# Kernel tuning notes

Hardware: AMD Instinct MI355X
Metric: run time of the kernel (lower is better)

Reference implementation:

```python
import jax, jax.numpy as jnp
import numpy as np

N, E, D, G, L = 100000, 1600000, 64, 512, 3
EPS = 1e-5


def setup_inputs() -> dict:
    key = jax.random.key(0)
    ks = jax.random.split(key, 8)
    x = jax.random.normal(ks[0], (N, D), dtype=jnp.float32)
    edge_index = jax.random.randint(ks[1], (2, E), 0, N, dtype=jnp.int32)
    batch = jnp.sort(jax.random.randint(ks[2], (N,), 0, G, dtype=jnp.int32))
    s = 1.0 / np.sqrt(D)
    convW = jax.random.normal(ks[3], (L, D, D), dtype=jnp.float32) * s
    convB = jnp.zeros((L, D), jnp.float32)
    bn_g = jnp.ones((L, D), jnp.float32); bn_b = jnp.zeros((L, D), jnp.float32)
    ln_g = jnp.ones((L, D), jnp.float32); ln_b = jnp.zeros((L, D), jnp.float32)
    W1 = jax.random.normal(ks[4], (3 * D, 2 * D), dtype=jnp.float32) * (1.0 / np.sqrt(3 * D))
    b1 = jnp.zeros((2 * D,), jnp.float32)
    ln1_g = jnp.ones((2 * D,), jnp.float32); ln1_b = jnp.zeros((2 * D,), jnp.float32)
    W2 = jax.random.normal(ks[5], (2 * D, D), dtype=jnp.float32) * (1.0 / np.sqrt(2 * D))
    b2 = jnp.zeros((D,), jnp.float32)
    ln2_g = jnp.ones((D,), jnp.float32); ln2_b = jnp.zeros((D,), jnp.float32)
    W3 = jax.random.normal(ks[6], (D, 1), dtype=jnp.float32) * s
    b3 = jnp.zeros((1,), jnp.float32)
    return dict(x=x, edge_index=edge_index, batch=batch, convW=convW, convB=convB,
                bn_g=bn_g, bn_b=bn_b, ln_g=ln_g, ln_b=ln_b,
                W1=W1, b1=b1, ln1_g=ln1_g, ln1_b=ln1_b,
                W2=W2, b2=b2, ln2_g=ln2_g, ln2_b=ln2_b, W3=W3, b3=b3)


def _layer_norm(h, g, b):
    mu = jnp.mean(h, axis=-1, keepdims=True)
    var = jnp.mean((h - mu) ** 2, axis=-1, keepdims=True)
    return (h - mu) * jax.lax.rsqrt(var + EPS) * g + b


def _forward(x, edge_index, batch, convW, convB, bn_g, bn_b, ln_g, ln_b,
             W1, b1, ln1_g, ln1_b, W2, b2, ln2_g, ln2_b, W3, b3):
    n = x.shape[0]
    loops = jnp.arange(n, dtype=edge_index.dtype)
    src = jnp.concatenate([edge_index[0], loops])  # self-loops as in GCNConv
    dst = jnp.concatenate([edge_index[1], loops])
    deg = jax.ops.segment_sum(jnp.ones_like(src, dtype=x.dtype), dst, num_segments=n)
    dinv = jnp.where(deg > 0, jax.lax.rsqrt(deg), 0.0)
    norm = (dinv[src] * dinv[dst])[:, None]  # [E+N, 1]

    h = x
    for i in range(L):
        x_in = h
        hw = h @ convW[i]                                   # [N, D]
        agg = jax.ops.segment_sum(norm * hw[src], dst, num_segments=n) + convB[i]
        # BatchNorm1d (train-mode batch stats, biased var)
        mu = jnp.mean(agg, axis=0)
        var = jnp.mean((agg - mu) ** 2, axis=0)
        hb = (agg - mu) * jax.lax.rsqrt(var + EPS) * bn_g[i] + bn_b[i]
        if i > 0:
            hb = hb + x_in  # residual (shapes match: D == D)
        h = jax.nn.gelu(_layer_norm(hb, ln_g[i], ln_b[i]), approximate=False)

    # multi-pool over graphs
    cnt = jax.ops.segment_sum(jnp.ones((n,), x.dtype), batch, num_segments=G)[:, None]
    s = jax.ops.segment_sum(h, batch, num_segments=G)
    mean = s / jnp.maximum(cnt, 1.0)
    mx = jax.ops.segment_max(h, batch, num_segments=G)
    mx = jnp.where(cnt > 0, mx, 0.0)
    z = jnp.concatenate([mean, mx, s], axis=1)  # [G, 3D]

    z = jax.nn.gelu(_layer_norm(z @ W1 + b1, ln1_g, ln1_b), approximate=False)
    z = jax.nn.gelu(_layer_norm(z @ W2 + b2, ln2_g, ln2_b), approximate=False)
    return z @ W3 + b3  # [G, num_classes]


def reference(x, edge_index, batch, convW, convB, bn_g, bn_b, ln_g, ln_b,
              W1, b1, ln1_g, ln1_b, W2, b2, ln2_g, ln2_b, W3, b3):
    return _forward(x, edge_index, batch, convW, convB, bn_g, bn_b, ln_g, ln_b,
                    W1, b1, ln1_g, ln1_b, W2, b2, ln2_g, ln2_b, W3, b3)
```

## Files before the change

kernel.cpp:

```cpp
#include <hip/hip_runtime.h>
#include <hip/hip_bf16.h>
#include <hip/hip_fp16.h>

#define DD 64
#define EPSV 1e-5f
#define NSLICE 16

typedef __attribute__((ext_vector_type(4))) _Float16 f16x4;
typedef __attribute__((ext_vector_type(8))) _Float16 f16x8;
typedef __attribute__((ext_vector_type(4))) float f32x4;

static __device__ __forceinline__ float fatomic_add(float* p, float v) {
#if defined(__HIP_DEVICE_COMPILE__)
    return unsafeAtomicAdd(p, v);
#else
    return 0.f;
#endif
}

static __device__ __forceinline__ float gelu_exact(float x) {
    return 0.5f * x * (1.0f + erff(x * 0.70710678118654752f));
}

static __device__ __forceinline__ void acc_u4(float* a8, uint4 v) {
    const __half2* hp = reinterpret_cast<const __half2*>(&v);
#pragma unroll
    for (int p = 0; p < 4; ++p) {
        float2 f = __half22float2(hp[p]);
        a8[2 * p] += f.x;
        a8[2 * p + 1] += f.y;
    }
}

#define ACHUNK 2048
#define NBMAX 400

__global__ __launch_bounds__(1024) void k_bcount(const int* __restrict__ dst,
                                                 int* __restrict__ bucketCnt,
                                                 int e, int nbuck) {
    __shared__ int h[NBMAX];
    int t = threadIdx.x;
    for (int i = t; i < nbuck; i += 1024) h[i] = 0;
    __syncthreads();
    int base = blockIdx.x * 8192;
#pragma unroll
    for (int k = 0; k < 8; ++k) {
        int i = base + k * 1024 + t;
        if (i < e) atomicAdd(&h[dst[i] >> 8], 1);
    }
    __syncthreads();
    for (int i = t; i < nbuck; i += 1024)
        if (h[i]) atomicAdd(&bucketCnt[i], h[i]);
}

__global__ __launch_bounds__(512) void k_bscan2(const int* __restrict__ bucketCnt,
                                                int* __restrict__ bbase,
                                                int* __restrict__ bcur,
                                                int* __restrict__ offs,
                                                int nbuck, int etotal, int n) {
    __shared__ int ws[8];
    int t = threadIdx.x, lane = t & 63, wv = t >> 6;
    int v = (t < nbuck) ? bucketCnt[t] : 0;
    int x = v;
#pragma unroll
    for (int o = 1; o < 64; o <<= 1) {
        int u = __shfl_up(x, o, 64);
        if (lane >= o) x += u;
    }
    if (lane == 63) ws[wv] = x;
    __syncthreads();
    int add = 0;
    for (int w = 0; w < wv; ++w) add += ws[w];
    int excl = add + x - v;
    if (t < nbuck) {
        bbase[t] = excl;
        bcur[t] = excl;
    }
    if (t == 0) {
        bbase[nbuck] = etotal;
        offs[n] = etotal;
    }
}

__global__ __launch_bounds__(1024) void k_dhist(const int* __restrict__ off,
                                                int* __restrict__ dcount, int n) {
    __shared__ int h[256];
    int t = threadIdx.x;
    if (t < 256) h[t] = 0;
    __syncthreads();
    int i = blockIdx.x * 1024 + t;
    if (i < n) {
        int d = min(off[i + 1] - off[i], 255);
        atomicAdd(&h[d], 1);
    }
    __syncthreads();
    if (t < 256 && h[t]) atomicAdd(&dcount[t], h[t]);
}

__global__ __launch_bounds__(256) void k_dscan(const int* __restrict__ dcount,
                                               int* __restrict__ dcur) {
    __shared__ int ws[4];
    int t = threadIdx.x;
    int lane = t & 63, wv = t >> 6;
    int v = dcount[t];
    int x = v;
#pragma unroll
    for (int o = 1; o < 64; o <<= 1) {
        int u = __shfl_up(x, o, 64);
        if (lane >= o) x += u;
    }
    if (lane == 63) ws[wv] = x;
    __syncthreads();
    int add = 0;
    for (int w = 0; w < wv; ++w) add += ws[w];
    dcur[t] = add + x - v;
}

__global__ __launch_bounds__(1024) void k_dscatter(const int* __restrict__ off,
                                                   int* __restrict__ dcur,
                                                   int* __restrict__ perm, int n) {
    __shared__ int lcnt[256], lbase[256];
    int t = threadIdx.x;
    if (t < 256) lcnt[t] = 0;
    __syncthreads();
    int i = blockIdx.x * 1024 + t;
    int d = 0, rank = 0;
    if (i < n) {
        d = min(off[i + 1] - off[i], 255);
        rank = atomicAdd(&lcnt[d], 1);
    }
    __syncthreads();
    if (t < 256 && lcnt[t]) lbase[t] = atomicAdd(&dcur[t], lcnt[t]);
    __syncthreads();
    if (i < n) perm[lbase[d] + rank] = i;
}

__global__ __launch_bounds__(256) void k_binA(const int* __restrict__ src,
                                              const int* __restrict__ dst,
                                              int* __restrict__ ebuf,
                                              int* __restrict__ bcur,
                                              int e, int nbuck) {
    __shared__ int cnt[NBMAX], startb[NBMAX], posb[NBMAX], gbase[NBMAX];
    __shared__ int stage[ACHUNK];
    __shared__ unsigned short stb[ACHUNK];
    int t = threadIdx.x;
    for (int cbase = blockIdx.x * ACHUNK; cbase < e; cbase += gridDim.x * ACHUNK) {
        int cval = min(ACHUNK, e - cbase);
        for (int i = t; i < nbuck; i += 256) { cnt[i] = 0; posb[i] = 0; }
        __syncthreads();
        int eb[8], es[8];
#pragma unroll
        for (int k = 0; k < 8; ++k) {
            int i = t + k * 256;
            if (i < cval) {
                int s = src[cbase + i];
                int d = dst[cbase + i];
                eb[k] = d >> 8;
                es[k] = s | ((d & 255) << 24);
                atomicAdd(&cnt[eb[k]], 1);
            } else eb[k] = -1;
        }
        __syncthreads();
        if (t == 0) {
            int r = 0;
            for (int b2 = 0; b2 < nbuck; ++b2) { startb[b2] = r; r += cnt[b2]; }
        }
        __syncthreads();
        for (int i = t; i < nbuck; i += 256)
            if (cnt[i] > 0) gbase[i] = atomicAdd(&bcur[i], cnt[i]);
#pragma unroll
        for (int k = 0; k < 8; ++k)
            if (eb[k] >= 0) {
                int idx = startb[eb[k]] + atomicAdd(&posb[eb[k]], 1);
                stage[idx] = es[k];
                stb[idx] = (unsigned short)eb[k];
            }
        __syncthreads();
        for (int i = t; i < cval; i += 256) {
            int b2 = stb[i];
            ebuf[gbase[b2] + (i - startb[b2])] = stage[i];
        }
        __syncthreads();
    }
}

__global__ __launch_bounds__(256) void k_binB(const int* __restrict__ ebuf,
                                              const int* __restrict__ bbase,
                                              int* __restrict__ offs,
                                              float* __restrict__ dinv,
                                              int* __restrict__ csr, int n) {
    __shared__ int cnt[256], cur[256], ws[4];
    int b = blockIdx.x;
    int base = b << 8;
    int nn = min(256, n - base);
    int t = threadIdx.x;
    int e0 = bbase[b], e1 = bbase[b + 1];
    cnt[t] = 0;
    __syncthreads();
    for (int i = e0 + t; i < e1; i += 256)
        atomicAdd(&cnt[((unsigned)ebuf[i]) >> 24], 1);
    __syncthreads();
    int v = cnt[t];
    int lane = t & 63, wv = t >> 6;
    int x = v;
#pragma unroll
    for (int o = 1; o < 64; o <<= 1) {
        int u = __shfl_up(x, o, 64);
        if (lane >= o) x += u;
    }
    if (lane == 63) ws[wv] = x;
    __syncthreads();
    int add = 0;
    for (int w = 0; w < wv; ++w) add += ws[w];
    int excl = add + x - v;
    if (t < nn) {
        offs[base + t] = e0 + excl;
        dinv[base + t] = rsqrtf((float)v + 1.0f);
    }
    cur[t] = e0 + excl;
    __syncthreads();
    for (int i = e0 + t; i < e1; i += 256) {
        int packed = ebuf[i];
        int dl = ((unsigned)packed) >> 24;
        int pos = atomicAdd(&cur[dl], 1);
        csr[pos] = packed & 0x00FFFFFF;
    }
}

__global__ void k_misc(const float* __restrict__ x, const float* __restrict__ dinv,
                       __half* __restrict__ mA, __half* __restrict__ mB, int n,
                       const int* __restrict__ batch, int* __restrict__ bnd, int g) {
    int i = blockIdx.x * 256 + threadIdx.x;
    int total = n * 64;
    if (i < total) {
        mA[i] = __float2half_rn(x[i] * dinv[i >> 6]);
    } else if (i < total + 64) {
        mA[i] = __float2half_rn(0.f);
        mB[i] = __float2half_rn(0.f);
    }
    if (i < n) {
        int b = batch[i];
        if (i == 0)
            for (int q = 0; q <= b; ++q) bnd[q] = 0;
        else {
            int pb = batch[i - 1];
            for (int q = pb + 1; q <= b; ++q) bnd[q] = i;
        }
        if (i == n - 1)
            for (int q = b + 1; q <= g; ++q) bnd[q] = n;
    }
}

__global__ __launch_bounds__(256, 4) void k_gather_gemm(const int* __restrict__ off,
                                                        const int* __restrict__ csr,
                                                        const float* __restrict__ dinv,
                                                        const __half* __restrict__ m16,
                                                        const float* __restrict__ W,
                                                        const float* __restrict__ convB,
                                                        const int* __restrict__ perm,
                                                        float* __restrict__ agg,
                                                        float* __restrict__ gstat,
                                                        int n, int nzero) {
    __shared__ float sred[128];
    const int t = threadIdx.x;
    const int lane = t & 63, wv = t >> 6;
    const int g = lane >> 4, ln = lane & 15;

    f16x8 bfr[2][4];
#pragma unroll
    for (int kt = 0; kt < 2; ++kt)
#pragma unroll
        for (int nt = 0; nt < 4; ++nt) {
            f16x8 h;
#pragma unroll
            for (int j = 0; j < 8; ++j)
                h[j] = (_Float16)W[(32 * kt + 8 * g + j) * 64 + 16 * nt + ln];
            bfr[kt][nt] = h;
        }

    if (t < 128) sred[t] = 0.f;
    __syncthreads();

    const int ntiles = (n + 15) >> 4;
    const int tile = blockIdx.x * 4 + wv;
    float s_acc[4] = {0.f, 0.f, 0.f, 0.f}, q_acc[4] = {0.f, 0.f, 0.f, 0.f};

    if (tile < ntiles) {
        const int slot = tile * 16 + ln;
        const bool valid = slot < n;
        const int node = valid ? perm[slot] : -1;
        const int row_self = valid ? node : nzero;
        int a = 0, deg = 0;
        float dd = 0.f;
        if (valid) {
            a = off[node];
            deg = off[node + 1] - a;
            dd = dinv[node];
        }
        int md = deg;
#pragma unroll
        for (int o = 1; o < 64; o <<= 1) md = max(md, __shfl_xor(md, o, 64));

        float acc[2][8];
#pragma unroll
        for (int kt = 0; kt < 2; ++kt)
#pragma unroll
            for (int j = 0; j < 8; ++j) acc[kt][j] = 0.f;

        const uint4* mrow4 = (const uint4*)m16;
        {
            const uint4* rp = mrow4 + ((size_t)row_self << 3) + g;
            uint4 v0 = rp[0], v1 = rp[4];
            acc_u4(acc[0], v0);
            acc_u4(acc[1], v1);
        }
        int ecur[4];
#pragma unroll
        for (int k = 0; k < 4; ++k) ecur[k] = (k < deg) ? csr[a + k] : nzero;
        for (int i = 0; i < md; i += 4) {
            int enx[4];
#pragma unroll
            for (int k = 0; k < 4; ++k) enx[k] = (i + 4 + k < deg) ? csr[a + i + 4 + k] : nzero;
            uint4 v[4][2];
#pragma unroll
            for (int r = 0; r < 4; ++r) {
                const uint4* rp = mrow4 + ((size_t)ecur[r] << 3) + g;
                v[r][0] = rp[0];
                v[r][1] = rp[4];
            }
#pragma unroll
            for (int r = 0; r < 4; ++r) {
                acc_u4(acc[0], v[r][0]);
                acc_u4(acc[1], v[r][1]);
            }
#pragma unroll
            for (int k = 0; k < 4; ++k) ecur[k] = enx[k];
        }

        f32x4 c[4];
#pragma unroll
        for (int nt = 0; nt < 4; ++nt) c[nt] = (f32x4){0.f, 0.f, 0.f, 0.f};
#pragma unroll
        for (int kt = 0; kt < 2; ++kt) {
            f16x8 ah, ar;
#pragma unroll
            for (int j = 0; j < 8; ++j) {
                float v = acc[kt][j] * dd;
                _Float16 h = (_Float16)v;
                ah[j] = h;
                ar[j] = (_Float16)(v - (float)h);
            }
#pragma unroll
            for (int nt = 0; nt < 4; ++nt) {
                c[nt] = __builtin_amdgcn_mfma_f32_16x16x32_f16(ah, bfr[kt][nt], c[nt], 0, 0, 0);
                c[nt] = __builtin_amdgcn_mfma_f32_16x16x32_f16(ar, bfr[kt][nt], c[nt], 0, 0, 0);
            }
        }

        int prow[4];
#pragma unroll
        for (int i = 0; i < 4; ++i) prow[i] = __shfl(node, 4 * g + i, 64);
        const float bias[4] = {convB[ln], convB[16 + ln], convB[32 + ln], convB[48 + ln]};
#pragma unroll
        for (int nt = 0; nt < 4; ++nt) {
#pragma unroll
            for (int i = 0; i < 4; ++i) {
                if (prow[i] >= 0) {
                    float v = c[nt][i] + bias[nt];
                    agg[(size_t)prow[i] * 64 + 16 * nt + ln] = v;
                    s_acc[nt] += v;
                    q_acc[nt] += v * v;
                }
            }
        }
#pragma unroll
        for (int nt = 0; nt < 4; ++nt) {
            s_acc[nt] += __shfl_xor(s_acc[nt], 16, 64);
            s_acc[nt] += __shfl_xor(s_acc[nt], 32, 64);
            q_acc[nt] += __shfl_xor(q_acc[nt], 16, 64);
            q_acc[nt] += __shfl_xor(q_acc[nt], 32, 64);
        }
        if (g == 0) {
#pragma unroll
            for (int nt = 0; nt < 4; ++nt) {
                atomicAdd(&sred[16 * nt + ln], s_acc[nt]);
                atomicAdd(&sred[64 + 16 * nt + ln], q_acc[nt]);
            }
        }
    }
    __syncthreads();
    if (t < 64) {
        float* gs = gstat + (blockIdx.x & (NSLICE - 1)) * 128;
        fatomic_add(&gs[t], sred[t]);
        fatomic_add(&gs[64 + t], sred[64 + t]);
    }
}

__global__ __launch_bounds__(256) void k_bn_ln_gelu(const float* __restrict__ agg,
                                                    const __half* __restrict__ m16res,
                                                    const float* __restrict__ gstat,
                                                    const float* __restrict__ dinv,
                                                    const float* __restrict__ bng,
                                                    const float* __restrict__ bnb,
                                                    const float* __restrict__ lng,
                                                    const float* __restrict__ lnb,
                                                    __half* __restrict__ m16out,
                                                    int n, int has_res, int scale_out) {
    int t = threadIdx.x;
    int lane = t & 63, wv = t >> 6;
    float fs = 0.f, fq = 0.f;
#pragma unroll
    for (int s = 0; s < NSLICE; ++s) {
        fs += gstat[s * 128 + lane];
        fq += gstat[s * 128 + 64 + lane];
    }
    float invN = 1.0f / (float)n;
    float mu_c = fs * invN;
    float var_c = fq * invN - mu_c * mu_c;
    float bscale = rsqrtf(var_c + EPSV) * bng[lane];
    float bshift = bnb[lane];
    float lg = lng[lane], lb = lnb[lane];
    for (int r = blockIdx.x * 4 + wv; r < n; r += gridDim.x * 4) {
        float dd = dinv[r];
        float x = agg[(size_t)r * 64 + lane];
        float hb = (x - mu_c) * bscale + bshift;
        if (has_res) hb += __half2float(m16res[(size_t)r * 64 + lane]) * (1.0f / dd);
        float ssum = hb;
#pragma unroll
        for (int off = 32; off; off >>= 1) ssum += __shfl_xor(ssum, off, 64);
        float rmu = ssum * (1.f / 64.f);
        float d = hb - rmu;
        float vs = d * d;
#pragma unroll
        for (int off = 32; off; off >>= 1) vs += __shfl_xor(vs, off, 64);
        float rvar = vs * (1.f / 64.f);
        float ln = d * rsqrtf(rvar + EPSV) * lg + lb;
        float g = gelu_exact(ln);
        float outv = scale_out ? g * dd : g;
        m16out[(size_t)r * 64 + lane] = __float2half_rn(outv);
    }
}

__global__ __launch_bounds__(256) void k_pool_z(const __half* __restrict__ h,
                                                const int* __restrict__ bnd,
                                                float* __restrict__ z) {
    int g = blockIdx.x;
    int t = threadIdx.x;
    int lane = t & 63, wv = t >> 6;
    int s0 = bnd[g], e0 = bnd[g + 1];
    float s = 0.f, mx = -INFINITY;
    for (int i = s0 + wv; i < e0; i += 4) {
        float v = __half2float(h[(size_t)i * 64 + lane]);
        s += v;
        mx = fmaxf(mx, v);
    }
    __shared__ float ss[256], sm[256];
    ss[t] = s;
    sm[t] = mx;
    __syncthreads();
    if (t < 64) {
        float fs = ss[t] + ss[t + 64] + ss[t + 128] + ss[t + 192];
        float fm = fmaxf(fmaxf(sm[t], sm[t + 64]), fmaxf(sm[t + 128], sm[t + 192]));
        float cntf = (float)(e0 - s0);
        float mean = fs / fmaxf(cntf, 1.0f);
        if (e0 == s0) fm = 0.f;
        z[g * 192 + t] = mean;
        z[g * 192 + 64 + t] = fm;
        z[g * 192 + 128 + t] = fs;
    }
}

__global__ __launch_bounds__(128) void k_head(const float* __restrict__ z,
                                              const float* __restrict__ W1, const float* __restrict__ b1,
                                              const float* __restrict__ ln1g, const float* __restrict__ ln1b,
                                              const float* __restrict__ W2, const float* __restrict__ b2,
                                              const float* __restrict__ ln2g, const float* __restrict__ ln2b,
                                              const float* __restrict__ W3, const float* __restrict__ b3,
                                              float* __restrict__ out) {
    int g = blockIdx.x;
    int t = threadIdx.x;
    int lane = t & 63, wv = t >> 6;
    __shared__ float zl[192], h1[128], red[2];
    for (int i = t; i < 192; i += 128) zl[i] = z[g * 192 + i];
    __syncthreads();
    float acc = b1[t];
    for (int k = 0; k < 192; ++k) acc += zl[k] * W1[k * 128 + t];
    float s = acc;
#pragma unroll
    for (int off = 32; off; off >>= 1) s += __shfl_xor(s, off, 64);
    if (lane == 0) red[wv] = s;
    __syncthreads();
    float mu = (red[0] + red[1]) * (1.f / 128.f);
    float d = acc - mu;
    float q = d * d;
#pragma unroll
    for (int off = 32; off; off >>= 1) q += __shfl_xor(q, off, 64);
    __syncthreads();
    if (lane == 0) red[wv] = q;
    __syncthreads();
    float var = (red[0] + red[1]) * (1.f / 128.f);
    float ln = d * rsqrtf(var + EPSV) * ln1g[t] + ln1b[t];
    h1[t] = gelu_exact(ln);
    __syncthreads();
    if (t < 64) {
        float acc2 = b2[t];
        for (int k = 0; k < 128; ++k) acc2 += h1[k] * W2[k * 64 + t];
        float s2 = acc2;
#pragma unroll
        for (int off = 32; off; off >>= 1) s2 += __shfl_xor(s2, off, 64);
        float mu2 = s2 * (1.f / 64.f);
        float d2 = acc2 - mu2;
        float q2 = d2 * d2;
#pragma unroll
        for (int off = 32; off; off >>= 1) q2 += __shfl_xor(q2, off, 64);
        float var2 = q2 * (1.f / 64.f);
        float l2 = d2 * rsqrtf(var2 + EPSV) * ln2g[t] + ln2b[t];
        float g2 = gelu_exact(l2);
        float p = g2 * W3[t];
#pragma unroll
        for (int off = 32; off; off >>= 1) p += __shfl_xor(p, off, 64);
        if (t == 0) out[g] = p + b3[0];
    }
}

extern "C" void kernel_launch(void* const* d_in, const int* in_sizes, int n_in,
                              void* d_out, int out_size, void* d_ws, size_t ws_size,
                              hipStream_t stream) {
    const float* x      = (const float*)d_in[0];
    const int*   eidx   = (const int*)d_in[1];
    const int*   batch  = (const int*)d_in[2];
    const float* convW  = (const float*)d_in[3];
    const float* convB  = (const float*)d_in[4];
    const float* bn_g   = (const float*)d_in[5];
    const float* bn_b   = (const float*)d_in[6];
    const float* ln_g   = (const float*)d_in[7];
    const float* ln_b   = (const float*)d_in[8];
    const float* W1     = (const float*)d_in[9];
    const float* b1     = (const float*)d_in[10];
    const float* ln1g   = (const float*)d_in[11];
    const float* ln1b   = (const float*)d_in[12];
    const float* W2     = (const float*)d_in[13];
    const float* b2     = (const float*)d_in[14];
    const float* ln2g   = (const float*)d_in[15];
    const float* ln2b   = (const float*)d_in[16];
    const float* W3     = (const float*)d_in[17];
    const float* b3     = (const float*)d_in[18];
    float* out = (float*)d_out;

    const int N = in_sizes[0] / DD;
    const int E = in_sizes[1] / 2;
    const int G = out_size;
    const int* esrc = eidx;
    const int* edst = eidx + E;

    char* ws = (char*)d_ws;
    size_t off_b = 0;
    auto alloc = [&](size_t bytes) {
        size_t p = off_b;
        off_b = (off_b + bytes + 255) & ~(size_t)255;
        return (void*)(ws + p);
    };
    int*    offs   = (int*)alloc((size_t)(N + 1) * 4);
    float*  dinv   = (float*)alloc((size_t)N * 4);
    int*    csr    = (int*)alloc((size_t)E * 4);
    int*    ebuf   = (int*)alloc((size_t)E * 4);
    __half* m16A   = (__half*)alloc((size_t)(N + 1) * DD * 2);
    __half* m16B   = (__half*)alloc((size_t)(N + 1) * DD * 2);
    float*  aggbuf = (float*)alloc((size_t)N * DD * 4);
    float*  gstats = (float*)alloc((size_t)3 * NSLICE * 128 * 4);
    int*    perm   = (int*)alloc((size_t)N * 4);
    int*    dcount = (int*)alloc(256 * 4);
    int*    dcur   = (int*)alloc(256 * 4);
    int*    bnd    = (int*)alloc((size_t)(G + 1) * 4);
    int*    bucketCnt = (int*)alloc((size_t)NBMAX * 4);
    int*    bbase  = (int*)alloc((size_t)(NBMAX + 1) * 4);
    int*    bcur   = (int*)alloc(((size_t)(N + 255) / 256) * 4);
    float* z = aggbuf;
    (void)ws_size; (void)n_in;

    const int nbuck = (N + 255) / 256;
    const int nb = (N + 1023) / 1024;

    hipMemsetAsync(gstats, 0, (size_t)3 * NSLICE * 128 * 4, stream);
    hipMemsetAsync(dcount, 0, 256 * 4, stream);
    hipMemsetAsync(bucketCnt, 0, (size_t)NBMAX * 4, stream);
    k_bcount<<<(E + 8191) / 8192, 1024, 0, stream>>>(edst, bucketCnt, E, nbuck);
    k_bscan2<<<1, 512, 0, stream>>>(bucketCnt, bbase, bcur, offs, nbuck, E, N);
    k_binA<<<(E + ACHUNK - 1) / ACHUNK, 256, 0, stream>>>(esrc, edst, ebuf, bcur, E, nbuck);
    k_binB<<<nbuck, 256, 0, stream>>>(ebuf, bbase, offs, dinv, csr, N);
    k_dhist<<<nb, 1024, 0, stream>>>(offs, dcount, N);
    k_dscan<<<1, 256, 0, stream>>>(dcount, dcur);
    k_dscatter<<<nb, 1024, 0, stream>>>(offs, dcur, perm, N);
    k_misc<<<((N + 1) * DD + 255) / 256, 256, 0, stream>>>(x, dinv, m16A, m16B, N, batch, bnd, G);

    __half* gin[3]  = {m16A, m16B, m16A};
    __half* gout[3] = {m16B, m16A, m16B};

    const int ntiles = (N + 15) / 16;
    const int gblocks = (ntiles + 3) / 4;

    for (int l = 0; l < 3; ++l) {
        float* gstat = gstats + (size_t)l * NSLICE * 128;
        k_gather_gemm<<<gblocks, 256, 0, stream>>>(offs, csr, dinv, (const __half*)gin[l],
                                                   convW + (size_t)l * DD * DD, convB + l * DD,
                                                   perm, aggbuf, gstat, N, N);
        k_bn_ln_gelu<<<2048, 256, 0, stream>>>(aggbuf, gin[l], gstat, dinv,
                                               bn_g + l * DD, bn_b + l * DD,
                                               ln_g + l * DD, ln_b + l * DD,
                                               gout[l], N, l > 0 ? 1 : 0, l < 2 ? 1 : 0);
    }

    k_pool_z<<<G, 256, 0, stream>>>(m16B, bnd, z);
    k_head<<<G, 128, 0, stream>>>(z, W1, b1, ln1g, ln1b, W2, b2, ln2g, ln2b, W3, b3, out);
}
```

Before: 418.6 us.

## Load-balance gather-GEMM tiles across waves using edge-weighted prefix ranges

Measured after the change: 421.3 us. About the same (+0.6%).

```diff
diff --git a/kernel.cpp b/kernel.cpp
--- a/kernel.cpp
+++ b/kernel.cpp
@@ -133,6 +133,78 @@
     if (t < 256 && lcnt[t]) lbase[t] = atomicAdd(&dcur[t], lcnt[t]);
     __syncthreads();
     if (i < n) perm[lbase[d] + rank] = i;
+}
+
+__global__ __launch_bounds__(1024) void k_slotinfo(const int* __restrict__ off,
+                                                   const float* __restrict__ dinv,
+                                                   const int* __restrict__ perm,
+                                                   int4* __restrict__ sinfo,
+                                                   int* __restrict__ tsum,
+                                                   int n, int ntiles) {
+    int s = blockIdx.x * 1024 + threadIdx.x;
+    int w = 0;
+    if (s < n) {
+        int node = perm[s];
+        int a = off[node];
+        int d = off[node + 1] - a;
+        sinfo[s] = make_int4(a, d, node, __float_as_int(dinv[node]));
+        w = d + 8;
+    } else if (s < ntiles * 16) {
+        sinfo[s] = make_int4(0, 0, -1, 0);
+    }
+    int lane = threadIdx.x & 63;
+#pragma unroll
+    for (int o = 1; o < 16; o <<= 1) w += __shfl_xor(w, o, 64);
+    if ((lane & 15) == 0 && s < ntiles * 16) tsum[s >> 4] = w;
+}
+
+__global__ __launch_bounds__(1024) void k_tscan(const int* __restrict__ tsum,
+                                                int* __restrict__ tprefix, int ntiles) {
+    __shared__ int wsum[16];
+    __shared__ int carry;
+    int t = threadIdx.x;
+    if (t == 0) carry = 0;
+    __syncthreads();
+    for (int base = 0; base < ntiles; base += 1024) {
+        int i = base + t;
+        int v = (i < ntiles) ? tsum[i] : 0;
+        int lane = t & 63, wv = t >> 6;
+        int x = v;
+#pragma unroll
+        for (int o = 1; o < 64; o <<= 1) {
+            int u = __shfl_up(x, o, 64);
+            if (lane >= o) x += u;
+        }
+        if (lane == 63) wsum[wv] = x;
+        __syncthreads();
+        int add = carry;
+        for (int w = 0; w < wv; ++w) add += wsum[w];
+        if (i < ntiles) tprefix[i] = add + x - v;
+        __syncthreads();
+        if (t == 0) {
+            int r = carry;
+            for (int w = 0; w < 16; ++w) r += wsum[w];
+            carry = r;
+        }
+        __syncthreads();
+    }
+    if (t == 0) tprefix[ntiles] = carry;
+}
+
+__global__ void k_wrange(const int* __restrict__ tprefix, int* __restrict__ wlo,
+                         int ntiles, int W) {
+    int w = blockIdx.x * 256 + threadIdx.x;
+    if (w > W) return;
+    if (w == W) { wlo[W] = ntiles; return; }
+    long total = tprefix[ntiles];
+    long T = (long)w * total / W;
+    int lo = 0, hi = ntiles;
+    while (lo < hi) {
+        int mid = (lo + hi) >> 1;
+        if ((long)tprefix[mid] < T) lo = mid + 1;
+        else hi = mid;
+    }
+    wlo[w] = lo;
 }
 
 __global__ __launch_bounds__(256) void k_binA(const int* __restrict__ src,
@@ -251,13 +323,12 @@
     }
 }
 
-__global__ __launch_bounds__(256, 4) void k_gather_gemm(const int* __restrict__ off,
+__global__ __launch_bounds__(256, 4) void k_gather_gemm(const int4* __restrict__ sinfo,
                                                         const int* __restrict__ csr,
-                                                        const float* __restrict__ dinv,
                                                         const __half* __restrict__ m16,
                                                         const float* __restrict__ W,
                                                         const float* __restrict__ convB,
-                                                        const int* __restrict__ perm,
+                                                        const int* __restrict__ wlo,
                                                         float* __restrict__ agg,
                                                         float* __restrict__ gstat,
                                                         int n, int nzero) {
@@ -277,26 +348,22 @@
                 h[j] = (_Float16)W[(32 * kt + 8 * g + j) * 64 + 16 * nt + ln];
             bfr[kt][nt] = h;
         }
+    const float bias[4] = {convB[ln], convB[16 + ln], convB[32 + ln], convB[48 + ln]};
 
     if (t < 128) sred[t] = 0.f;
     __syncthreads();
 
-    const int ntiles = (n + 15) >> 4;
-    const int tile = blockIdx.x * 4 + wv;
+    const int wvid = blockIdx.x * 4 + wv;
+    const int lo = wlo[wvid], hi = wlo[wvid + 1];
     float s_acc[4] = {0.f, 0.f, 0.f, 0.f}, q_acc[4] = {0.f, 0.f, 0.f, 0.f};
-
-    if (tile < ntiles) {
-        const int slot = tile * 16 + ln;
-        const bool valid = slot < n;
-        const int node = valid ? perm[slot] : -1;
-        const int row_self = valid ? node : nzero;
-        int a = 0, deg = 0;
-        float dd = 0.f;
-        if (valid) {
-            a = off[node];
-            deg = off[node + 1] - a;
-            dd = dinv[node];
-        }
+    const uint4* mrow4 = (const uint4*)m16;
+
+    for (int tile = lo; tile < hi; ++tile) {
+        const int4 si = sinfo[tile * 16 + ln];
+        const int a = si.x, deg = si.y, node = si.z;
+        const float dd = __int_as_float(si.w);
+        const int row_self = (node >= 0) ? node : nzero;
+
         int md = deg;
 #pragma unroll
         for (int o = 1; o < 64; o <<= 1) md = max(md, __shfl_xor(md, o, 64));
@@ -307,7 +374,6 @@
 #pragma unroll
             for (int j = 0; j < 8; ++j) acc[kt][j] = 0.f;
 
-        const uint4* mrow4 = (const uint4*)m16;
         {
             const uint4* rp = mrow4 + ((size_t)row_self << 3) + g;
             uint4 v0 = rp[0], v1 = rp[4];
@@ -360,7 +426,6 @@
         int prow[4];
 #pragma unroll
         for (int i = 0; i < 4; ++i) prow[i] = __shfl(node, 4 * g + i, 64);
-        const float bias[4] = {convB[ln], convB[16 + ln], convB[32 + ln], convB[48 + ln]};
 #pragma unroll
         for (int nt = 0; nt < 4; ++nt) {
 #pragma unroll
@@ -373,19 +438,20 @@
                 }
             }
         }
+    }
+
+#pragma unroll
+    for (int nt = 0; nt < 4; ++nt) {
+        s_acc[nt] += __shfl_xor(s_acc[nt], 16, 64);
+        s_acc[nt] += __shfl_xor(s_acc[nt], 32, 64);
+        q_acc[nt] += __shfl_xor(q_acc[nt], 16, 64);
+        q_acc[nt] += __shfl_xor(q_acc[nt], 32, 64);
+    }
+    if (g == 0) {
 #pragma unroll
         for (int nt = 0; nt < 4; ++nt) {
-            s_acc[nt] += __shfl_xor(s_acc[nt], 16, 64);
-            s_acc[nt] += __shfl_xor(s_acc[nt], 32, 64);
-            q_acc[nt] += __shfl_xor(q_acc[nt], 16, 64);
-            q_acc[nt] += __shfl_xor(q_acc[nt], 32, 64);
-        }
-        if (g == 0) {
-#pragma unroll
-            for (int nt = 0; nt < 4; ++nt) {
-                atomicAdd(&sred[16 * nt + ln], s_acc[nt]);
-                atomicAdd(&sred[64 + 16 * nt + ln], q_acc[nt]);
-            }
+            atomicAdd(&sred[16 * nt + ln], s_acc[nt]);
+            atomicAdd(&sred[64 + 16 * nt + ln], q_acc[nt]);
         }
     }
     __syncthreads();
@@ -560,6 +626,10 @@
         off_b = (off_b + bytes + 255) & ~(size_t)255;
         return (void*)(ws + p);
     };
+    const int ntiles = (N + 15) / 16;
+    const int gblocks = (ntiles + 3) / 4;
+    const int NW = gblocks * 4;
+
     int*    offs   = (int*)alloc((size_t)(N + 1) * 4);
     float*  dinv   = (float*)alloc((size_t)N * 4);
     int*    csr    = (int*)alloc((size_t)E * 4);
@@ -569,6 +639,10 @@
     float*  aggbuf = (float*)alloc((size_t)N * DD * 4);
     float*  gstats = (float*)alloc((size_t)3 * NSLICE * 128 * 4);
     int*    perm   = (int*)alloc((size_t)N * 4);
+    int4*   sinfo  = (int4*)alloc((size_t)ntiles * 16 * 16);
+    int*    tsum   = (int*)alloc((size_t)ntiles * 4);
+    int*    tprefix= (int*)alloc((size_t)(ntiles + 1) * 4);
+    int*    wlo    = (int*)alloc((size_t)(NW + 1) * 4);
     int*    dcount = (int*)alloc(256 * 4);
     int*    dcur   = (int*)alloc(256 * 4);
     int*    bnd    = (int*)alloc((size_t)(G + 1) * 4);
@@ -591,19 +665,20 @@
     k_dhist<<<nb, 1024, 0, stream>>>(offs, dcount, N);
     k_dscan<<<1, 256, 0, stream>>>(dcount, dcur);
     k_dscatter<<<nb, 1024, 0, stream>>>(offs, dcur, perm, N);
+    k_slotinfo<<<(ntiles * 16 + 1023) / 1024, 1024, 0, stream>>>(offs, dinv, perm, sinfo,
+                                                                 tsum, N, ntiles);
+    k_tscan<<<1, 1024, 0, stream>>>(tsum, tprefix, ntiles);
+    k_wrange<<<(NW + 256) / 256, 256, 0, stream>>>(tprefix, wlo, ntiles, NW);
     k_misc<<<((N + 1) * DD + 255) / 256, 256, 0, stream>>>(x, dinv, m16A, m16B, N, batch, bnd, G);
 
     __half* gin[3]  = {m16A, m16B, m16A};
     __half* gout[3] = {m16B, m16A, m16B};
 
-    const int ntiles = (N + 15) / 16;
-    const int gblocks = (ntiles + 3) / 4;
-
     for (int l = 0; l < 3; ++l) {
         float* gstat = gstats + (size_t)l * NSLICE * 128;
-        k_gather_gemm<<<gblocks, 256, 0, stream>>>(offs, csr, dinv, (const __half*)gin[l],
+        k_gather_gemm<<<gblocks, 256, 0, stream>>>(sinfo, csr, (const __half*)gin[l],
                                                    convW + (size_t)l * DD * DD, convB + l * DD,
-                                                   perm, aggbuf, gstat, N, N);
+                                                   wlo, aggbuf, gstat, N, N);
         k_bn_ln_gelu<<<2048, 256, 0, stream>>>(aggbuf, gin[l], gstat, dinv,
                                                bn_g + l * DD, bn_b + l * DD,
                                                ln_g + l * DD, ln_b + l * DD,
```
